# Kernel tuning notes

Hardware: AMD Instinct MI355X
Metric: run time of the kernel (lower is better)

The kernel has to match this reference:

```python
import jax, jax.numpy as jnp
import numpy as np

N_NODES = 100000
N_EDGES = 1600000
D_IN = 128
D_OUT = 128
EPS = 1e-5


def setup_inputs() -> dict:
    key = jax.random.key(0)
    k1, k2, k3, k4, k5 = jax.random.split(key, 5)
    x = jax.random.normal(k1, (N_NODES, D_IN), dtype=jnp.float32)
    row = jax.random.randint(k2, (N_EDGES,), 0, N_NODES, dtype=jnp.int64)
    col = jax.random.randint(k3, (N_EDGES,), 0, N_NODES, dtype=jnp.int64)
    adj_vals = jax.random.uniform(k4, (N_EDGES,), dtype=jnp.float32)
    # Xavier-uniform init for weight, zeros for bias (as in the torch module)
    limit = float(np.sqrt(6.0 / (D_IN + D_OUT)))
    weight = jax.random.uniform(k5, (D_IN, D_OUT), minval=-limit, maxval=limit, dtype=jnp.float32)
    bias = jnp.zeros((D_OUT,), dtype=jnp.float32)
    return {"x": x, "row": row, "col": col, "adj_vals": adj_vals, "weight": weight, "bias": bias}


def reference(x, row, col, adj_vals, weight, bias):
    # degree = row-sum of sparse adj
    degree = jax.ops.segment_sum(adj_vals, row, num_segments=N_NODES)
    degree = jnp.where(degree == 0, EPS, degree)
    d_inv_sqrt = (degree + EPS) ** -0.5  # [N]
    # edge-wise symmetric normalization: D^-1/2 A D^-1/2
    edge_w = d_inv_sqrt[row] * adj_vals * d_inv_sqrt[col]  # [E]
    # SpMM: gather neighbor features, scale, scatter-add to destination rows
    msgs = edge_w[:, None] * x[col]  # [E, D_IN]
    agg = jax.ops.segment_sum(msgs, row, num_segments=N_NODES)  # [N, D_IN]
    return agg @ weight + bias
```

## Files before the change

### kernel.cpp

```cpp
#include <hip/hip_runtime.h>

#define NN 100000
#define NE 1600000
#define D  128
#define EPS 1e-5f

#define NBKT   782
#define NEB    391
#define EPB_H  4096
#define GRID_G 782
#define NSCAN  (NBKT*NEB)
#define GRID2  299
#define CAP    2560

#define OFF_HCNT 0x0000000ULL
#define OFF_PART 0x0140000ULL
#define OFF_BASE 0x0142000ULL
#define OFF_DINV 0x0150000ULL
#define OFF_GREC 0x0200000ULL
#define OFF_YB   0x0F00000ULL

typedef short short8 __attribute__((ext_vector_type(8)));
typedef float f32x4 __attribute__((ext_vector_type(4)));

static __device__ __forceinline__ unsigned f2bf(float f) {
    unsigned u = __float_as_uint(f);
    return (u + 0x7fffu + ((u >> 16) & 1u)) >> 16;
}

__launch_bounds__(256, 2)
__global__ void k1(const float* __restrict__ x, const float* __restrict__ w,
                   const int* __restrict__ row,
                   unsigned* __restrict__ hcnt, unsigned short* __restrict__ yb) {
    __shared__ unsigned short sx[128 * 128];
    __shared__ unsigned short sw[128 * 128];
    int tid = threadIdx.x;
    int bid = blockIdx.x;

    if (bid < NEB) {
        unsigned* h = (unsigned*)sx;
        for (int i = tid; i < NBKT; i += 256) h[i] = 0;
        __syncthreads();
        int ebeg = bid * EPB_H;
        for (int i = tid; i < EPB_H; i += 256) {
            int e = ebeg + i;
            if (e < NE) atomicAdd(&h[((unsigned)row[e]) >> 7], 1u);
        }
        __syncthreads();
        for (int i = tid; i < NBKT; i += 256) hcnt[i * NEB + bid] = h[i];
        return;
    }

    int base = (bid - NEB) * 128;
    const float* wmat = w;

    #pragma unroll
    for (int i = 0; i < 8; ++i) {
        int task = i * 256 + tid;
        int n = task & 127, ko = task >> 7;
        const float* wp = wmat + (size_t)(ko * 8) * D + n;
        uint4 pk;
        pk.x = f2bf(wp[0])     | (f2bf(wp[D])     << 16);
        pk.y = f2bf(wp[2 * D]) | (f2bf(wp[3 * D]) << 16);
        pk.z = f2bf(wp[4 * D]) | (f2bf(wp[5 * D]) << 16);
        pk.w = f2bf(wp[6 * D]) | (f2bf(wp[7 * D]) << 16);
        int idx = (n * 128 + ko * 8) ^ ((n & 7) << 3);
        *(uint4*)(&sw[idx]) = pk;
    }
    #pragma unroll
    for (int i = 0; i < 8; ++i) {
        int task = i * 256 + tid;
        int ko = task & 15, r = task >> 4;
        int gr = base + r;
        float4 f0 = make_float4(0.f, 0.f, 0.f, 0.f), f1 = f0;
        if (gr < NN) {
            const float* xp = x + (size_t)gr * D + ko * 8;
            f0 = *(const float4*)xp;
            f1 = *(const float4*)(xp + 4);
        }
        uint4 pk;
        pk.x = f2bf(f0.x) | (f2bf(f0.y) << 16);
        pk.y = f2bf(f0.z) | (f2bf(f0.w) << 16);
        pk.z = f2bf(f1.x) | (f2bf(f1.y) << 16);
        pk.w = f2bf(f1.z) | (f2bf(f1.w) << 16);
        int idx = (r * 128 + ko * 8) ^ ((r & 7) << 3);
        *(uint4*)(&sx[idx]) = pk;
    }
    __syncthreads();

    int wv = tid >> 6, l = tid & 63;
    int lr = l & 15, g = l >> 4;

    f32x4 acc[2][8];
    #pragma unroll
    for (int ti = 0; ti < 2; ++ti)
        #pragma unroll
        for (int tj = 0; tj < 8; ++tj)
            acc[ti][tj] = (f32x4){0.f, 0.f, 0.f, 0.f};

    #pragma unroll
    for (int kc = 0; kc < 4; ++kc) {
        int kb = kc * 32 + g * 8;
        short8 a[2], b[8];
        #pragma unroll
        for (int ti = 0; ti < 2; ++ti) {
            int r0 = wv * 32 + ti * 16 + lr;
            a[ti] = *(const short8*)(&sx[(r0 * 128 + kb) ^ ((r0 & 7) << 3)]);
        }
        #pragma unroll
        for (int tj = 0; tj < 8; ++tj) {
            int n0 = tj * 16 + lr;
            b[tj] = *(const short8*)(&sw[(n0 * 128 + kb) ^ ((n0 & 7) << 3)]);
        }
        #pragma unroll
        for (int ti = 0; ti < 2; ++ti)
            #pragma unroll
            for (int tj = 0; tj < 8; ++tj)
                acc[ti][tj] = __builtin_amdgcn_mfma_f32_16x16x32_bf16(
                    a[ti], b[tj], acc[ti][tj], 0, 0, 0);
    }

    #pragma unroll
    for (int ti = 0; ti < 2; ++ti) {
        #pragma unroll
        for (int reg = 0; reg < 4; ++reg) {
            int gr = base + wv * 32 + ti * 16 + g * 4 + reg;
            if (gr < NN) {
                #pragma unroll
                for (int tj = 0; tj < 8; ++tj)
                    yb[(size_t)gr * D + tj * 16 + lr] = (unsigned short)f2bf(acc[ti][tj][reg]);
            }
        }
    }
}

__global__ void k2a(const unsigned* __restrict__ hcnt, unsigned* __restrict__ part) {
    __shared__ unsigned s[256];
    int t = threadIdx.x;
    int gi = blockIdx.x * 1024 + t * 4;
    unsigned v = 0;
    #pragma unroll
    for (int j = 0; j < 4; ++j) if (gi + j < NSCAN) v += hcnt[gi + j];
    s[t] = v;
    __syncthreads();
    for (int d = 128; d > 0; d >>= 1) {
        if (t < d) s[t] += s[t + d];
        __syncthreads();
    }
    if (t == 0) part[blockIdx.x] = s[0];
}

__launch_bounds__(512)
__global__ void k2b(const unsigned* __restrict__ part, unsigned* __restrict__ base) {
    __shared__ unsigned s[512];
    int t = threadIdx.x;
    unsigned v = (t < GRID2) ? part[t] : 0;
    s[t] = v;
    __syncthreads();
    for (int d = 1; d < 512; d <<= 1) {
        unsigned u = (t >= d) ? s[t - d] : 0;
        __syncthreads();
        s[t] += u;
        __syncthreads();
    }
    if (t < GRID2) base[t] = s[t] - v;
}

__global__ void k2c(unsigned* __restrict__ hcnt, const unsigned* __restrict__ base) {
    __shared__ unsigned s[256];
    int t = threadIdx.x;
    int gi = blockIdx.x * 1024 + t * 4;
    unsigned v[4], tot = 0;
    #pragma unroll
    for (int j = 0; j < 4; ++j) {
        v[j] = (gi + j < NSCAN) ? hcnt[gi + j] : 0;
        tot += v[j];
    }
    s[t] = tot;
    __syncthreads();
    for (int d = 1; d < 256; d <<= 1) {
        unsigned u = (t >= d) ? s[t - d] : 0;
        __syncthreads();
        s[t] += u;
        __syncthreads();
    }
    unsigned run = base[blockIdx.x] + s[t] - tot;
    #pragma unroll
    for (int j = 0; j < 4; ++j) {
        if (gi + j < NSCAN) { hcnt[gi + j] = run; run += v[j]; }
    }
}

__launch_bounds__(256)
__global__ void k3(const int* __restrict__ row, const int* __restrict__ col,
                   const float* __restrict__ adj, const unsigned* __restrict__ hcnt,
                   unsigned long long* __restrict__ grec) {
    __shared__ unsigned cur[NBKT];
    int t = threadIdx.x, b = blockIdx.x;
    for (int i = t; i < NBKT; i += 256) cur[i] = hcnt[i * NEB + b];
    __syncthreads();
    int ebeg = b * EPB_H;
    for (int i = t; i < EPB_H; i += 256) {
        int e = ebeg + i;
        if (e >= NE) continue;
        unsigned r = (unsigned)row[e];
        unsigned aq = (unsigned)rintf(adj[e] * 32767.0f);
        unsigned lo = (unsigned)col[e] | (aq << 17);
        unsigned dst = atomicAdd(&cur[r >> 7], 1u);
        grec[dst] = (unsigned long long)lo | ((unsigned long long)(r & 127u) << 32);
    }
}

__global__ void k4a(const unsigned* __restrict__ hcnt, const unsigned long long* __restrict__ grec,
                    float* __restrict__ dinv) {
    __shared__ unsigned s[128];
    int t = threadIdx.x, b = blockIdx.x;
    if (t < 128) s[t] = 0;
    __syncthreads();
    unsigned beg = hcnt[b * NEB];
    unsigned end = (b == NBKT - 1) ? NE : hcnt[(b + 1) * NEB];
    for (unsigned p = beg + t; p < end; p += 256) {
        unsigned long long rec = grec[p];
        atomicAdd(&s[(unsigned)(rec >> 32) & 127u], ((unsigned)rec >> 17) & 0x7FFFu);
    }
    __syncthreads();
    if (t < 128) {
        int r = b * 128 + t;
        if (r < NN) {
            float d = (float)s[t] * (1.0f / 32767.0f);
            d = (d == 0.0f) ? EPS : d;
            dinv[r] = rsqrtf(d + EPS);
        }
    }
}

__launch_bounds__(256, 4)
__global__ void k4b(const unsigned* __restrict__ hcnt, const unsigned long long* __restrict__ grec,
                    const float* __restrict__ dinv, const unsigned short* __restrict__ yb,
                    const float* __restrict__ bias, float* __restrict__ out) {
    __shared__ unsigned ecol[CAP + 8];
    __shared__ unsigned cnt[128], rb[128], cur[128], sc[128];
    int t = threadIdx.x, b = blockIdx.x;

    if (t < 128) cnt[t] = 0;
    __syncthreads();
    unsigned beg = hcnt[b * NEB];
    unsigned end = (b == NBKT - 1) ? NE : hcnt[(b + 1) * NEB];
    for (unsigned p = beg + t; p < end; p += 256)
        atomicAdd(&cnt[(unsigned)(grec[p] >> 32) & 127u], 1u);
    __syncthreads();

    if (t < 128) sc[t] = cnt[t];
    __syncthreads();
    for (int d = 1; d < 128; d <<= 1) {
        unsigned u = (t >= d && t < 128) ? sc[t - d] : 0;
        __syncthreads();
        if (t < 128) sc[t] += u;
        __syncthreads();
    }
    if (t < 128) { rb[t] = sc[t] - cnt[t]; cur[t] = sc[t] - cnt[t]; }
    __syncthreads();

    for (unsigned p = beg + t; p < end; p += 256) {
        unsigned long long rec = grec[p];
        unsigned rank = atomicAdd(&cur[(unsigned)(rec >> 32) & 127u], 1u);
        if (rank < CAP) ecol[rank] = (unsigned)rec;
    }
    __syncthreads();

    int grp = t >> 4, lq = t & 15;
    for (int k = 0; k < 8; ++k) {
        int rowlo = grp * 8 + k;
        int r = b * 128 + rowlo;
        if (r >= NN) continue;
        unsigned jb = rb[rowlo];
        unsigned c  = cnt[rowlo];
        unsigned jend = min(jb + c, (unsigned)CAP);

        float a0 = 0.f, a1 = 0.f, a2 = 0.f, a3 = 0.f;
        float a4 = 0.f, a5 = 0.f, a6 = 0.f, a7 = 0.f;

        for (unsigned j = jb; j < jend; j += 8) {
            unsigned ee[8];
            uint4 yq[8];
            float wv[8];
            int cm[8];
            #pragma unroll
            for (int u = 0; u < 8; ++u) ee[u] = ecol[j + u];
            #pragma unroll
            for (int u = 0; u < 8; ++u) cm[u] = min((int)(ee[u] & 0x1FFFFu), NN - 1);
            #pragma unroll
            for (int u = 0; u < 8; ++u)
                yq[u] = ((const uint4*)(yb + (size_t)cm[u] * D))[lq];
            #pragma unroll
            for (int u = 0; u < 8; ++u)
                wv[u] = (j + u < jend) ? (float)(ee[u] >> 17) * dinv[cm[u]] : 0.f;
            #pragma unroll
            for (int u = 0; u < 8; ++u) {
                a0 += wv[u] * __uint_as_float(yq[u].x << 16);
                a1 += wv[u] * __uint_as_float(yq[u].x & 0xffff0000u);
                a2 += wv[u] * __uint_as_float(yq[u].y << 16);
                a3 += wv[u] * __uint_as_float(yq[u].y & 0xffff0000u);
                a4 += wv[u] * __uint_as_float(yq[u].z << 16);
                a5 += wv[u] * __uint_as_float(yq[u].z & 0xffff0000u);
                a6 += wv[u] * __uint_as_float(yq[u].w << 16);
                a7 += wv[u] * __uint_as_float(yq[u].w & 0xffff0000u);
            }
        }

        float scale = dinv[r] * (1.0f / 32767.0f);
        const float4* bp = (const float4*)bias + lq * 2;
        float4* op = (float4*)(out + (size_t)r * D) + lq * 2;
        float4 b0 = bp[0], b1 = bp[1];
        op[0] = make_float4(a0 * scale + b0.x, a1 * scale + b0.y,
                            a2 * scale + b0.z, a3 * scale + b0.w);
        op[1] = make_float4(a4 * scale + b1.x, a5 * scale + b1.y,
                            a6 * scale + b1.z, a7 * scale + b1.w);
    }
}

extern "C" void kernel_launch(void* const* d_in, const int* in_sizes, int n_in,
                              void* d_out, int out_size, void* d_ws, size_t ws_size,
                              hipStream_t stream) {
    const float* x    = (const float*)d_in[0];
    const int*   row  = (const int*)d_in[1];
    const int*   col  = (const int*)d_in[2];
    const float* adj  = (const float*)d_in[3];
    const float* wgt  = (const float*)d_in[4];
    const float* bias = (const float*)d_in[5];
    float* out = (float*)d_out;
    char*  ws  = (char*)d_ws;

    unsigned* hcnt = (unsigned*)(ws + OFF_HCNT);
    unsigned* part = (unsigned*)(ws + OFF_PART);
    unsigned* basep= (unsigned*)(ws + OFF_BASE);
    float*    dinv = (float*)(ws + OFF_DINV);
    unsigned long long* grec = (unsigned long long*)(ws + OFF_GREC);
    unsigned short* yb = (unsigned short*)(ws + OFF_YB);

    k1 <<<NEB + GRID_G, 256, 0, stream>>>(x, wgt, row, hcnt, yb);
    k2a<<<GRID2, 256, 0, stream>>>(hcnt, part);
    k2b<<<1, 512, 0, stream>>>(part, basep);
    k2c<<<GRID2, 256, 0, stream>>>(hcnt, basep);
    k3 <<<NEB, 256, 0, stream>>>(row, col, adj, hcnt, grec);
    k4a<<<NBKT, 256, 0, stream>>>(hcnt, grec, dinv);
    k4b<<<NBKT, 256, 0, stream>>>(hcnt, grec, dinv, yb, bias, out);
}
```

Baseline: 148.6 us.

## Split histogram from GEMM kernel and stage bucket records in shared memory

Splits the fused histogram+bf16 GEMM kernel into two separate launches, so the histogram blocks no longer carry the GEMM's 64KB shared allocation and its occupancy limit. In the aggregation kernel, bucket records read during the counting pass are also kept in a shared-memory buffer and reused for the scatter pass, avoiding a second global read of grec. This costs one extra launch and about 20KB more shared memory per block in k4b, which can lower its occupancy.

Measured after the change: 149.0 us. No clear change (+0.3%).

```diff
diff --git a/kernel.cpp b/kernel.cpp
--- a/kernel.cpp
+++ b/kernel.cpp
@@ -28,37 +28,33 @@
     return (u + 0x7fffu + ((u >> 16) & 1u)) >> 16;
 }
 
+__global__ void k0h(const int* __restrict__ row, unsigned* __restrict__ hcnt) {
+    __shared__ unsigned h[NBKT];
+    int t = threadIdx.x, b = blockIdx.x;
+    for (int i = t; i < NBKT; i += 256) h[i] = 0;
+    __syncthreads();
+    int ebeg = b * EPB_H;
+    for (int i = t; i < EPB_H; i += 256) {
+        int e = ebeg + i;
+        if (e < NE) atomicAdd(&h[((unsigned)row[e]) >> 7], 1u);
+    }
+    __syncthreads();
+    for (int i = t; i < NBKT; i += 256) hcnt[i * NEB + b] = h[i];
+}
+
 __launch_bounds__(256, 2)
-__global__ void k1(const float* __restrict__ x, const float* __restrict__ w,
-                   const int* __restrict__ row,
-                   unsigned* __restrict__ hcnt, unsigned short* __restrict__ yb) {
+__global__ void k1g(const float* __restrict__ x, const float* __restrict__ w,
+                    unsigned short* __restrict__ yb) {
     __shared__ unsigned short sx[128 * 128];
     __shared__ unsigned short sw[128 * 128];
     int tid = threadIdx.x;
-    int bid = blockIdx.x;
-
-    if (bid < NEB) {
-        unsigned* h = (unsigned*)sx;
-        for (int i = tid; i < NBKT; i += 256) h[i] = 0;
-        __syncthreads();
-        int ebeg = bid * EPB_H;
-        for (int i = tid; i < EPB_H; i += 256) {
-            int e = ebeg + i;
-            if (e < NE) atomicAdd(&h[((unsigned)row[e]) >> 7], 1u);
-        }
-        __syncthreads();
-        for (int i = tid; i < NBKT; i += 256) hcnt[i * NEB + bid] = h[i];
-        return;
-    }
-
-    int base = (bid - NEB) * 128;
-    const float* wmat = w;
+    int base = blockIdx.x * 128;
 
     #pragma unroll
     for (int i = 0; i < 8; ++i) {
         int task = i * 256 + tid;
         int n = task & 127, ko = task >> 7;
-        const float* wp = wmat + (size_t)(ko * 8) * D + n;
+        const float* wp = w + (size_t)(ko * 8) * D + n;
         uint4 pk;
         pk.x = f2bf(wp[0])     | (f2bf(wp[D])     << 16);
         pk.y = f2bf(wp[2 * D]) | (f2bf(wp[3 * D]) << 16);
@@ -238,6 +234,7 @@
 __global__ void k4b(const unsigned* __restrict__ hcnt, const unsigned long long* __restrict__ grec,
                     const float* __restrict__ dinv, const unsigned short* __restrict__ yb,
                     const float* __restrict__ bias, float* __restrict__ out) {
+    __shared__ unsigned long long srec[CAP];
     __shared__ unsigned ecol[CAP + 8];
     __shared__ unsigned cnt[128], rb[128], cur[128], sc[128];
     int t = threadIdx.x, b = blockIdx.x;
@@ -246,8 +243,12 @@
     __syncthreads();
     unsigned beg = hcnt[b * NEB];
     unsigned end = (b == NBKT - 1) ? NE : hcnt[(b + 1) * NEB];
-    for (unsigned p = beg + t; p < end; p += 256)
-        atomicAdd(&cnt[(unsigned)(grec[p] >> 32) & 127u], 1u);
+    unsigned n = end - beg;
+    for (unsigned i = t; i < n; i += 256) {
+        unsigned long long rec = grec[beg + i];
+        if (i < CAP) srec[i] = rec;
+        atomicAdd(&cnt[(unsigned)(rec >> 32) & 127u], 1u);
+    }
     __syncthreads();
 
     if (t < 128) sc[t] = cnt[t];
@@ -261,8 +262,9 @@
     if (t < 128) { rb[t] = sc[t] - cnt[t]; cur[t] = sc[t] - cnt[t]; }
     __syncthreads();
 
-    for (unsigned p = beg + t; p < end; p += 256) {
-        unsigned long long rec = grec[p];
+    unsigned ns = min(n, (unsigned)CAP);
+    for (unsigned i = t; i < ns; i += 256) {
+        unsigned long long rec = srec[i];
         unsigned rank = atomicAdd(&cur[(unsigned)(rec >> 32) & 127u], 1u);
         if (rank < CAP) ecol[rank] = (unsigned)rec;
     }
@@ -331,14 +333,15 @@
     float* out = (float*)d_out;
     char*  ws  = (char*)d_ws;
 
-    unsigned* hcnt = (unsigned*)(ws + OFF_HCNT);
-    unsigned* part = (unsigned*)(ws + OFF_PART);
-    unsigned* basep= (unsigned*)(ws + OFF_BASE);
-    float*    dinv = (float*)(ws + OFF_DINV);
+    unsigned* hcnt  = (unsigned*)(ws + OFF_HCNT);
+    unsigned* part  = (unsigned*)(ws + OFF_PART);
+    unsigned* basep = (unsigned*)(ws + OFF_BASE);
+    float*    dinv  = (float*)(ws + OFF_DINV);
     unsigned long long* grec = (unsigned long long*)(ws + OFF_GREC);
     unsigned short* yb = (unsigned short*)(ws + OFF_YB);
 
-    k1 <<<NEB + GRID_G, 256, 0, stream>>>(x, wgt, row, hcnt, yb);
+    k0h<<<NEB, 256, 0, stream>>>(row, hcnt);
+    k1g<<<GRID_G, 256, 0, stream>>>(x, wgt, yb);
     k2a<<<GRID2, 256, 0, stream>>>(hcnt, part);
     k2b<<<1, 512, 0, stream>>>(part, basep);
     k2c<<<GRID2, 256, 0, stream>>>(hcnt, basep);
```
